# Performance work log

Hardware: AMD Instinct MI355X
Metric: run time of the kernel (lower is better)

Reference implementation:

```python
import jax, jax.numpy as jnp
import numpy as np

S = 4096; V = 50257; E = 1024; H = 1024; T = 1024  # seq, vocab, embed, hidden, tagset (tagset must == hidden)


def setup_inputs() -> dict:
    key = jax.random.key(0)
    ks = jax.random.split(key, 10)
    return {
        "sentence": jax.random.randint(ks[0], (S,), 0, V),
        "emb": jax.random.normal(ks[1], (V, E), jnp.float32) * 0.02,
        "W_ih": jax.random.normal(ks[2], (4 * H, E), jnp.float32) * 0.03,  # torch nn.LSTM weight_ih_l0, gate order i,f,g,o
        "W_hh": jax.random.normal(ks[3], (4 * H, H), jnp.float32) * 0.03,
        "b_ih": jax.random.normal(ks[4], (4 * H,), jnp.float32) * 0.01,
        "b_hh": jax.random.normal(ks[5], (4 * H,), jnp.float32) * 0.01,
        "W_tag": jax.random.normal(ks[6], (T, H), jnp.float32) * 0.03,
        "b_tag": jnp.zeros((T,), jnp.float32),
        "W_hyb": jax.random.normal(ks[7], (1, T), jnp.float32) * 0.03,
        "b_hyb": jnp.zeros((1,), jnp.float32),
    }


def _lstm_tags(sentence, emb, W_ih, W_hh, b_ih, b_hh, W_tag, b_tag, W_hyb, b_hyb):
    x = emb[sentence]                       # [S, E] embedding lookup (batch=1 squeezed)
    # precompute input contribution for all timesteps in one GEMM: [S, 4H]
    x_gates = x @ W_ih.T + (b_ih + b_hh)

    def step(carry, xg):
        h, c = carry                        # [H], [H]
        gates = xg + W_hh @ h               # [4H]
        i, f, g, o = jnp.split(gates, 4)
        i = jax.nn.sigmoid(i); f = jax.nn.sigmoid(f)
        g = jnp.tanh(g);       o = jax.nn.sigmoid(o)
        c = f * c + i * g
        h = o * jnp.tanh(c)
        return (h, c), h

    init = (jnp.zeros((H,), x.dtype), jnp.zeros((H,), x.dtype))
    _, hs = jax.lax.scan(step, init, x_gates)  # hs: [S, H]
    tag_logits = hs @ W_tag.T + b_tag          # [S, T]
    # Hybrid head: sigmoid(linear(tag_logits) + shift), shift = 0
    return jax.nn.sigmoid(tag_logits @ W_hyb.T + b_hyb)  # [S, 1]


def reference(sentence, emb, W_ih, W_hh, b_ih, b_hh, W_tag, b_tag, W_hyb, b_hyb):
    return _lstm_tags(sentence, emb, W_ih, W_hh, b_ih, b_hh, W_tag, b_tag, W_hyb, b_hyb)
```

## Files before the change

### kernel.cpp

```cpp
#include <hip/hip_runtime.h>
#include <hip/hip_bf16.h>
#include <cstdint>

#define SEQ   4096
#define EDIM  1024
#define HDIM  1024
#define G4H   4096
#define NBLK  64

typedef __attribute__((ext_vector_type(8))) short short8;
typedef __attribute__((ext_vector_type(4))) float f32x4;

__device__ inline unsigned short f2bf(float f) {
    __bf16 b = (__bf16)f;
    return __builtin_bit_cast(unsigned short, b);
}


__global__ __launch_bounds__(256) void conv_wih(const float* __restrict__ w,
                                                unsigned short* __restrict__ o) {
    size_t i = ((size_t)blockIdx.x * 256 + threadIdx.x) * 4;
    float4 v = *reinterpret_cast<const float4*>(w + i);
    ushort4 u;
    u.x = f2bf(v.x); u.y = f2bf(v.y); u.z = f2bf(v.z); u.w = f2bf(v.w);
    *reinterpret_cast<ushort4*>(o + i) = u;
}

__global__ __launch_bounds__(256) void gather_x(const int* __restrict__ sent,
                                                const float* __restrict__ emb,
                                                unsigned short* __restrict__ xo) {
    int s = blockIdx.x;
    int idx = sent[s];
    int i = threadIdx.x * 4;
    float4 v = *reinterpret_cast<const float4*>(emb + (size_t)idx * EDIM + i);
    ushort4 u;
    u.x = f2bf(v.x); u.y = f2bf(v.y); u.z = f2bf(v.z); u.w = f2bf(v.w);
    *reinterpret_cast<ushort4*>(xo + (size_t)s * EDIM + i) = u;
}

__global__ __launch_bounds__(256) void weff_kernel(const float* __restrict__ wtag,
                                                   const float* __restrict__ btag,
                                                   const float* __restrict__ whyb,
                                                   const float* __restrict__ bhyb,
                                                   float* __restrict__ weff) {
    if (blockIdx.x < 4) {
        int hcol = blockIdx.x * 256 + threadIdx.x;
        float acc = 0.f;
        #pragma unroll 8
        for (int t = 0; t < 1024; ++t)
            acc += whyb[t] * wtag[(size_t)t * HDIM + hcol];
        weff[hcol] = acc;
    } else {
        __shared__ float red[256];
        float acc = 0.f;
        for (int t = threadIdx.x; t < 1024; t += 256) acc += whyb[t] * btag[t];
        red[threadIdx.x] = acc;
        __syncthreads();
        for (int s2 = 128; s2 > 0; s2 >>= 1) {
            if ((int)threadIdx.x < s2) red[threadIdx.x] += red[threadIdx.x + s2];
            __syncthreads();
        }
        if (threadIdx.x == 0) weff[1024] = red[0] + bhyb[0];
    }
}


__global__ __launch_bounds__(256) void gemm_xgates(const unsigned short* __restrict__ xbf,
                                                   const unsigned short* __restrict__ wihbf,
                                                   const float* __restrict__ b_ih,
                                                   const float* __restrict__ b_hh,
                                                   float* __restrict__ xg) {
    __shared__ short A_l[128 * 64];
    __shared__ short B_l[128 * 64];
    const int tid  = threadIdx.x;
    const int lane = tid & 63;
    const int wid  = tid >> 6;
    const int wm = wid >> 1, wn = wid & 1;
    const int bm = blockIdx.x * 128, bn = blockIdx.y * 128;

    f32x4 acc[4][4];
    #pragma unroll
    for (int mt = 0; mt < 4; ++mt)
        #pragma unroll
        for (int nt = 0; nt < 4; ++nt) {
            f32x4 z = {0.f, 0.f, 0.f, 0.f};
            acc[mt][nt] = z;
        }

    for (int ks = 0; ks < EDIM / 64; ++ks) {
        uint4 ta[4], tb[4];
        #pragma unroll
        for (int r = 0; r < 4; ++r) {
            int lin = r * 256 + tid;
            int row = lin >> 3;
            int kc  = lin & 7;
            const unsigned short* ga = xbf   + (size_t)(bm + row) * EDIM + ks * 64 + kc * 8;
            const unsigned short* gb = wihbf + (size_t)(bn + row) * EDIM + ks * 64 + kc * 8;
            ta[r] = *reinterpret_cast<const uint4*>(ga);
            tb[r] = *reinterpret_cast<const uint4*>(gb);
        }
        __syncthreads();
        #pragma unroll
        for (int r = 0; r < 4; ++r) {
            int lin = r * 256 + tid;
            *reinterpret_cast<uint4*>(&A_l[lin * 8]) = ta[r];
            *reinterpret_cast<uint4*>(&B_l[lin * 8]) = tb[r];
        }
        __syncthreads();
        #pragma unroll
        for (int kk = 0; kk < 2; ++kk) {
            short8 af[4], bfr[4];
            #pragma unroll
            for (int mt = 0; mt < 4; ++mt) {
                int row = wm * 64 + mt * 16 + (lane & 15);
                af[mt] = *reinterpret_cast<const short8*>(&A_l[row * 64 + kk * 32 + (lane >> 4) * 8]);
            }
            #pragma unroll
            for (int nt = 0; nt < 4; ++nt) {
                int row = wn * 64 + nt * 16 + (lane & 15);
                bfr[nt] = *reinterpret_cast<const short8*>(&B_l[row * 64 + kk * 32 + (lane >> 4) * 8]);
            }
            #pragma unroll
            for (int mt = 0; mt < 4; ++mt)
                #pragma unroll
                for (int nt = 0; nt < 4; ++nt)
                    acc[mt][nt] = __builtin_amdgcn_mfma_f32_16x16x32_bf16(af[mt], bfr[nt], acc[mt][nt], 0, 0, 0);
        }
    }
    #pragma unroll
    for (int nt = 0; nt < 4; ++nt) {
        int gn = bn + wn * 64 + nt * 16 + (lane & 15);
        float bias = b_ih[gn] + b_hh[gn];
        #pragma unroll
        for (int mt = 0; mt < 4; ++mt) {
            int gm0 = bm + wm * 64 + mt * 16 + (lane >> 4) * 4;
            #pragma unroll
            for (int r = 0; r < 4; ++r)
                xg[(size_t)(gm0 + r) * G4H + gn] = acc[mt][nt][r] + bias;
        }
    }
}


__global__ __launch_bounds__(512, 2) void lstm_seq(const float* __restrict__ xg,
                                                   const float* __restrict__ whh,
                                                   unsigned long long* __restrict__ hglob,
                                                   float* __restrict__ hs)
{
    const int tid  = threadIdx.x;
    const int b    = blockIdx.x;
    const int lane = tid & 63;
    const int wv   = tid >> 6;

    __shared__ float hlds[1024];
    __shared__ float gsm[64];
    __shared__ float xgs[2][64];

    float4 w[8][4];
    #pragma unroll
    for (int rr = 0; rr < 8; ++rr) {
        int rl = wv * 8 + rr;
        int grow = ((rl >> 4) << 10) + (b << 4) + (rl & 15);
        #pragma unroll
        for (int q = 0; q < 4; ++q)
            w[rr][q] = *reinterpret_cast<const float4*>(whh + (size_t)grow * HDIM + lane * 16 + q * 4);
    }

    if (wv == 1) {
        int grow = ((lane >> 4) << 10) + (b << 4) + (lane & 15);
        xgs[0][lane] = xg[grow];
    }

    float c = 0.f;

    for (int t = 0; t < SEQ; ++t) {
        if (wv == 0) {
            const unsigned long long* src = hglob + (size_t)(t & 1) * HDIM;
            unsigned long long u[16];
            for (;;) {
                bool ok = true;
                #pragma unroll
                for (int i = 0; i < 16; ++i) {
                    u[i] = __hip_atomic_load(src + i * 64 + lane, __ATOMIC_RELAXED,
                                             __HIP_MEMORY_SCOPE_AGENT);
                    ok &= ((unsigned)(u[i] >> 32) >= (unsigned)t);
                }
                if (__all(ok)) break;
            }
            #pragma unroll
            for (int i = 0; i < 16; ++i)
                hlds[i * 64 + lane] = __builtin_bit_cast(float, (unsigned)(u[i] & 0xffffffffu));
        } else if (wv == 1) {
            if (t + 1 < SEQ) {
                int grow = ((lane >> 4) << 10) + (b << 4) + (lane & 15);
                xgs[(t + 1) & 1][lane] = xg[(size_t)(t + 1) * G4H + grow];
            }
        }
        __syncthreads();

        float4 h4[4];
        #pragma unroll
        for (int q = 0; q < 4; ++q)
            h4[q] = *reinterpret_cast<const float4*>(&hlds[lane * 16 + q * 4]);
        float p[8];
        #pragma unroll
        for (int rr = 0; rr < 8; ++rr) {
            float s = 0.f;
            #pragma unroll
            for (int q = 0; q < 4; ++q)
                s += w[rr][q].x * h4[q].x + w[rr][q].y * h4[q].y
                   + w[rr][q].z * h4[q].z + w[rr][q].w * h4[q].w;
            p[rr] = s;
        }
        #pragma unroll
        for (int m = 1; m < 64; m <<= 1) {
            #pragma unroll
            for (int rr = 0; rr < 8; ++rr)
                p[rr] += __shfl_xor(p[rr], m);
        }
        if (lane == 0) {
            #pragma unroll
            for (int rr = 0; rr < 8; ++rr)
                gsm[wv * 8 + rr] = p[rr] + xgs[t & 1][wv * 8 + rr];
        }
        __syncthreads();

        if (tid < 16) {
            float gi = gsm[tid], gf = gsm[16 + tid], gg = gsm[32 + tid], go = gsm[48 + tid];
            float iv = 1.f / (1.f + __expf(-gi));
            float fv = 1.f / (1.f + __expf(-gf));
            float e2 = __expf(2.f * gg);
            float gv = (e2 - 1.f) / (e2 + 1.f);
            float ov = 1.f / (1.f + __expf(-go));
            c = fv * c + iv * gv;
            float e2c = __expf(2.f * c);
            float hn = ov * ((e2c - 1.f) / (e2c + 1.f));
            hs[(size_t)t * HDIM + (b << 4) + tid] = hn;
            unsigned long long pk = ((unsigned long long)(unsigned)(t + 1) << 32)
                                  | (unsigned long long)__builtin_bit_cast(unsigned, hn);
            __hip_atomic_store(hglob + (size_t)((t + 1) & 1) * HDIM + (b << 4) + tid, pk,
                               __ATOMIC_RELAXED, __HIP_MEMORY_SCOPE_AGENT);
        }
    }
}


__global__ __launch_bounds__(256) void out_head(const float* __restrict__ hs,
                                                const float* __restrict__ weff,
                                                float* __restrict__ out) {
    int wid = threadIdx.x >> 6, lane = threadIdx.x & 63;
    int s = blockIdx.x * 4 + wid;
    const float* h = hs + (size_t)s * HDIM;
    float sum = 0.f;
    #pragma unroll
    for (int i = 0; i < 4; ++i) {
        float4 hv = *reinterpret_cast<const float4*>(h + i * 256 + lane * 4);
        float4 wv = *reinterpret_cast<const float4*>(weff + i * 256 + lane * 4);
        sum += hv.x * wv.x + hv.y * wv.y + hv.z * wv.z + hv.w * wv.w;
    }
    #pragma unroll
    for (int m = 1; m < 64; m <<= 1) sum += __shfl_xor(sum, m);
    if (lane == 0) out[s] = 1.f / (1.f + __expf(-(sum + weff[1024])));
}


extern "C" void kernel_launch(void* const* d_in, const int* in_sizes, int n_in,
                              void* d_out, int out_size, void* d_ws, size_t ws_size,
                              hipStream_t stream) {
    const int*   sent = (const int*)d_in[0];
    const float* emb  = (const float*)d_in[1];
    const float* wih  = (const float*)d_in[2];
    const float* whh  = (const float*)d_in[3];
    const float* bih  = (const float*)d_in[4];
    const float* bhh  = (const float*)d_in[5];
    const float* wtag = (const float*)d_in[6];
    const float* btag = (const float*)d_in[7];
    const float* whyb = (const float*)d_in[8];
    const float* bhyb = (const float*)d_in[9];
    float* out = (float*)d_out;

    char* ws = (char*)d_ws;
    float*              xg    = (float*)(ws);
    float*              hs    = (float*)(ws + ((size_t)64 << 20));
    unsigned short*     xbf   = (unsigned short*)(ws + ((size_t)80 << 20));
    unsigned short*     wihbf = (unsigned short*)(ws + ((size_t)88 << 20));
    float*              weff  = (float*)(ws + ((size_t)96 << 20));
    unsigned long long* hglob = (unsigned long long*)(ws + ((size_t)96 << 20) + 8192);

    (void)hipMemsetAsync(hglob, 0, 2 * HDIM * sizeof(unsigned long long), stream);

    conv_wih<<<4096, 256, 0, stream>>>(wih, wihbf);
    gather_x<<<4096, 256, 0, stream>>>(sent, emb, xbf);
    weff_kernel<<<5, 256, 0, stream>>>(wtag, btag, whyb, bhyb, weff);

    dim3 gg(32, 32);
    gemm_xgates<<<gg, 256, 0, stream>>>(xbf, wihbf, bih, bhh, xg);

    void* args[] = { (void*)&xg, (void*)&whh, (void*)&hglob, (void*)&hs };
    (void)hipLaunchCooperativeKernel((const void*)lstm_seq, dim3(NBLK), dim3(512),
                                     args, 0, stream);

    out_head<<<1024, 256, 0, stream>>>(hs, weff, out);
}
```

Baseline: 11.34 ms.

## Have every wave poll h directly from global and shrink the reduction tree

Each wave now spins on the global hidden-state buffer itself, with each lane loading its own 16 contiguous entries. This removes the LDS staging buffer and one __syncthreads per timestep. The cross-lane reduction is reworked so the 8 row sums are transposed into lanes after 3 shuffle stages, cutting shuffles from 48 to 24 per wave. The xg prefetch moves into per-lane registers. The risk is 8x more global polling traffic per block, and uncoalesced per-lane loads of 16 contiguous 8-byte words.

New measurement: 25.75 ms. 127% more time.

```diff
diff --git a/kernel.cpp b/kernel.cpp
--- a/kernel.cpp
+++ b/kernel.cpp
@@ -152,76 +152,86 @@
     const int lane = tid & 63;
     const int wv   = tid >> 6;
 
-    __shared__ float hlds[1024];
     __shared__ float gsm[64];
-    __shared__ float xgs[2][64];
-
-    float4 w[8][4];
+
+    float w_[8][16];
     #pragma unroll
     for (int rr = 0; rr < 8; ++rr) {
-        int rl = wv * 8 + rr;
+        int rl   = wv * 8 + rr;
         int grow = ((rl >> 4) << 10) + (b << 4) + (rl & 15);
         #pragma unroll
-        for (int q = 0; q < 4; ++q)
-            w[rr][q] = *reinterpret_cast<const float4*>(whh + (size_t)grow * HDIM + lane * 16 + q * 4);
-    }
-
-    if (wv == 1) {
-        int grow = ((lane >> 4) << 10) + (b << 4) + (lane & 15);
-        xgs[0][lane] = xg[grow];
-    }
+        for (int q = 0; q < 4; ++q) {
+            float4 v = *reinterpret_cast<const float4*>(whh + (size_t)grow * HDIM + lane * 16 + q * 4);
+            w_[rr][q * 4 + 0] = v.x;
+            w_[rr][q * 4 + 1] = v.y;
+            w_[rr][q * 4 + 2] = v.z;
+            w_[rr][q * 4 + 3] = v.w;
+        }
+    }
+    #pragma unroll
+    for (int rr = 0; rr < 8; ++rr)
+        #pragma unroll
+        for (int k = 0; k < 16; ++k)
+            asm volatile("" : "+v"(w_[rr][k]));
+
+    const int myrow  = wv * 8 + lane;
+    const int mygrow = ((myrow >> 4) << 10) + (b << 4) + (myrow & 15);
+    float xg_next = 0.f;
+    if (lane < 8) xg_next = xg[mygrow];
 
     float c = 0.f;
 
     for (int t = 0; t < SEQ; ++t) {
-        if (wv == 0) {
-            const unsigned long long* src = hglob + (size_t)(t & 1) * HDIM;
-            unsigned long long u[16];
-            for (;;) {
-                bool ok = true;
-                #pragma unroll
-                for (int i = 0; i < 16; ++i) {
-                    u[i] = __hip_atomic_load(src + i * 64 + lane, __ATOMIC_RELAXED,
-                                             __HIP_MEMORY_SCOPE_AGENT);
-                    ok &= ((unsigned)(u[i] >> 32) >= (unsigned)t);
-                }
-                if (__all(ok)) break;
+        float xg_cur = xg_next;
+        if (lane < 8 && t + 1 < SEQ)
+            xg_next = xg[(size_t)(t + 1) * G4H + mygrow];
+
+        const unsigned long long* src = hglob + (size_t)(t & 1) * HDIM + (lane << 4);
+        while ((unsigned)(__hip_atomic_load(src, __ATOMIC_RELAXED,
+                                            __HIP_MEMORY_SCOPE_AGENT) >> 32) < (unsigned)t) {}
+        unsigned long long u[16];
+        bool ok;
+        do {
+            ok = true;
+            #pragma unroll
+            for (int k = 0; k < 16; ++k) {
+                u[k] = __hip_atomic_load(src + k, __ATOMIC_RELAXED,
+                                         __HIP_MEMORY_SCOPE_AGENT);
+                ok &= ((unsigned)(u[k] >> 32) >= (unsigned)t);
             }
-            #pragma unroll
-            for (int i = 0; i < 16; ++i)
-                hlds[i * 64 + lane] = __builtin_bit_cast(float, (unsigned)(u[i] & 0xffffffffu));
-        } else if (wv == 1) {
-            if (t + 1 < SEQ) {
-                int grow = ((lane >> 4) << 10) + (b << 4) + (lane & 15);
-                xgs[(t + 1) & 1][lane] = xg[(size_t)(t + 1) * G4H + grow];
-            }
-        }
-        __syncthreads();
-
-        float4 h4[4];
-        #pragma unroll
-        for (int q = 0; q < 4; ++q)
-            h4[q] = *reinterpret_cast<const float4*>(&hlds[lane * 16 + q * 4]);
+        } while (!ok);
+
+        float h_[16];
+        #pragma unroll
+        for (int k = 0; k < 16; ++k)
+            h_[k] = __builtin_bit_cast(float, (unsigned)(u[k] & 0xffffffffu));
+
         float p[8];
         #pragma unroll
         for (int rr = 0; rr < 8; ++rr) {
             float s = 0.f;
             #pragma unroll
-            for (int q = 0; q < 4; ++q)
-                s += w[rr][q].x * h4[q].x + w[rr][q].y * h4[q].y
-                   + w[rr][q].z * h4[q].z + w[rr][q].w * h4[q].w;
+            for (int k = 0; k < 16; ++k) s += w_[rr][k] * h_[k];
             p[rr] = s;
         }
         #pragma unroll
-        for (int m = 1; m < 64; m <<= 1) {
-            #pragma unroll
-            for (int rr = 0; rr < 8; ++rr)
-                p[rr] += __shfl_xor(p[rr], m);
-        }
-        if (lane == 0) {
-            #pragma unroll
-            for (int rr = 0; rr < 8; ++rr)
-                gsm[wv * 8 + rr] = p[rr] + xgs[t & 1][wv * 8 + rr];
+        for (int m = 1; m < 8; m <<= 1) {
+            #pragma unroll
+            for (int rr = 0; rr < 8; ++rr) p[rr] += __shfl_xor(p[rr], m);
+        }
+        {
+            const int sel = lane & 7;
+            float a0 = (sel & 1) ? p[1] : p[0];
+            float a1 = (sel & 1) ? p[3] : p[2];
+            float a2 = (sel & 1) ? p[5] : p[4];
+            float a3 = (sel & 1) ? p[7] : p[6];
+            float b0 = (sel & 2) ? a1 : a0;
+            float b1 = (sel & 2) ? a3 : a2;
+            float q  = (sel & 4) ? b1 : b0;
+            q += __shfl_xor(q, 8);
+            q += __shfl_xor(q, 16);
+            q += __shfl_xor(q, 32);
+            if (lane < 8) gsm[wv * 8 + lane] = q + xg_cur;
         }
         __syncthreads();
 
```
